# Kernel optimization log

Measured on AMD Instinct MI355X. Metric: run time of the kernel, lower is better.

The kernel has to match this reference:

```python
import jax, jax.numpy as jnp
import numpy as np

TESS = 5  # number of cells
N_POINTS = 16_777_216


def _make_basis(nc):
    # Continuity constraints of piecewise-affine velocity v(x)=a_c x + b_c at
    # interior knots x_i = i/nc:  a_i x_i + b_i - a_{i+1} x_i - b_{i+1} = 0.
    L = np.zeros((nc - 1, 2 * nc), dtype=np.float64)
    for i in range(1, nc):
        xb = i / nc
        L[i - 1, 2 * (i - 1)] = xb
        L[i - 1, 2 * (i - 1) + 1] = 1.0
        L[i - 1, 2 * i] = -xb
        L[i - 1, 2 * i + 1] = -1.0
    _, _, Vt = np.linalg.svd(L)
    B = Vt[nc - 1:].T  # (2*nc, nc+1) orthonormal null-space basis ('svd')
    return B.astype(np.float32)


def setup_inputs() -> dict:
    key = jax.random.key(0)
    k1, k2 = jax.random.split(key)
    x = jax.random.uniform(k1, (N_POINTS,), dtype=jnp.float32)
    theta = jax.random.normal(k2, (1, TESS + 1), dtype=jnp.float32) * 0.5
    B = jnp.asarray(_make_basis(TESS))
    return {"x": x, "theta": theta, "B": B}


def reference(x, theta, B):
    EPS = 1e-7
    TINY = 1e-12
    BIG = 1e10
    nc = B.shape[0] // 2
    x = jnp.clip(x, EPS, 1.0 - EPS)
    A = (B @ theta[0]).reshape(nc, 2)  # per-cell affine velocity [a_c, b_c]
    a_all, b_all = A[:, 0], A[:, 1]
    c0 = jnp.clip(jnp.floor(x * nc), 0, nc - 1).astype(jnp.int32)

    def step(carry, _):
        xc, c, t, logder = carry
        a = a_all[c]
        b = b_all[c]
        v = a * xc + b
        big = jnp.abs(a) > 1e-8
        sa = jnp.where(big, a, 1.0)
        eat = jnp.exp(a * t)
        # exact in-cell ODE solution psi(x, t)
        psi = jnp.where(big, xc * eat + (b / sa) * (eat - 1.0), xc + b * t)
        right = v >= 0
        xb = jnp.where(right, (c + 1).astype(xc.dtype), c.astype(xc.dtype)) / nc
        den = xc + b / sa
        sden = jnp.where(jnp.abs(den) > TINY, den, TINY)
        ratio = (xb + b / sa) / sden
        thit_a = jnp.log(jnp.maximum(ratio, TINY)) / sa  # time to reach boundary
        sb = jnp.where(jnp.abs(b) > TINY, b, TINY)
        thit_b = (xb - xc) / sb
        thit = jnp.where(big, thit_a, thit_b)
        valid = (jnp.abs(v) > TINY) & (thit >= 0.0) & jnp.where(big, ratio > 0.0, True)
        thit = jnp.where(valid, thit, BIG)
        hits = thit < t
        dt = jnp.where(hits, thit, t)
        x_new = jnp.where(hits, xb, psi)
        c_new = jnp.where(hits, jnp.clip(c + jnp.where(right, 1, -1), 0, nc - 1), c)
        return (x_new, c_new, t - dt, logder + a * dt), None

    init = (x, c0, jnp.ones_like(x), jnp.zeros_like(x))
    (z, _, _, logder), _ = jax.lax.scan(step, init, None, length=nc + 2)
    # log(dz/dx) = sum_c a_c * dt_c  (derivative of flow is exp of integrated slope)
    return z, logder
```

## Files before the change

### kernel.cpp

```cpp
#include <hip/hip_runtime.h>

#define NC 5
#define VEC 4


__global__ void setup_kernel(const float* __restrict__ theta,
                             const float* __restrict__ B,
                             float* __restrict__ ws)
{
    const int tid = threadIdx.x;
    const float TINY = 1e-12f, BIG = 1e10f;

    float a[NC], b[NC], bosa[NC], isa[NC], isbv[NC];
    #pragma unroll
    for (int c = 0; c < NC; ++c) {
        float av = 0.f, bv = 0.f;
        #pragma unroll
        for (int j = 0; j < 6; ++j) {
            float th = theta[j];
            av = fmaf(B[(2 * c) * 6 + j], th, av);
            bv = fmaf(B[(2 * c + 1) * 6 + j], th, bv);
        }
        const bool  big = fabsf(av) > 1e-8f;
        const float sa  = big ? av : 1.0f;
        const float sb  = (fabsf(bv) > TINY) ? bv : TINY;
        a[c] = av; b[c] = bv;
        bosa[c] = bv / sa;
        isa[c]  = 1.0f / sa;
        isbv[c] = 1.0f / sb;
    }

    if (tid < NC) {
        ws[tid * 4 + 0] = a[tid];
        ws[tid * 4 + 1] = b[tid];
        ws[tid * 4 + 2] = bosa[tid];
        ws[tid * 4 + 3] = isa[tid];
        ws[20 + tid]    = isbv[tid];
    }
    if (tid < 6) ws[25 + tid] = (float)tid / 5.0f;

    if (tid < 12) {
        const int d  = tid / 6;
        const int jb = tid % 6;
        float Ccum = 0.f, Lcum = 0.f;
        float th0 = BIG, th1 = BIG, th2 = BIG, th3 = BIG;

        for (int m = 0; m < 5; ++m) {
            const int  cf   = (d == 0) ? (jb + m) : (jb - 1 - m);
            const bool sent = (cf < 0) || (cf >= NC);
            const float xe  = (d == 0) ? ((float)cf / 5.0f)
                                       : ((float)(cf + 1) / 5.0f);
            const float af    = sent ? 0.f : a[cf];
            const float bf    = sent ? 0.f : b[cf];
            const float bosaf = sent ? 0.f : bosa[cf];

            const int pix = tid * 5 + m;
            ws[ 80 + pix * 4 + 0] = Ccum;
            ws[ 80 + pix * 4 + 1] = Lcum;
            ws[ 80 + pix * 4 + 2] = xe;
            ws[ 80 + pix * 4 + 3] = af;
            ws[320 + pix * 4 + 0] = bf;
            ws[320 + pix * 4 + 1] = bosaf;
            ws[320 + pix * 4 + 2] = 0.f;
            ws[320 + pix * 4 + 3] = 0.f;

            float T = BIG;
            if (!sent) {
                const float xL  = (float)cf / 5.0f;
                const float xR  = (float)(cf + 1) / 5.0f;
                const float xce = (d == 0) ? xL : xR;
                const float xbt = (d == 0) ? xR : xL;
                const float v   = fmaf(af, xce, bf);
                const bool  big = fabsf(af) > 1e-8f;
                const float den  = xce + bosaf;
                const float sden = (fabsf(den) > TINY) ? den : TINY;
                const float ratio = __fdividef(xbt + bosaf, sden);
                const float ta = __logf(fmaxf(ratio, TINY)) * isa[cf];
                const float tb = (xbt - xce) * isbv[cf];
                float thit = big ? ta : tb;
                const bool valid = (fabsf(v) > TINY) && (thit >= 0.f) &&
                                   (!big || (ratio > 0.f));
                T = valid ? thit : BIG;
            }
            const float newC = Ccum + T;
            if (m == 0) th0 = newC;
            if (m == 1) th1 = newC;
            if (m == 2) th2 = newC;
            if (m == 3) th3 = newC;
            if (T < BIG) Lcum = fmaf(af, T, Lcum);
            Ccum = newC;
        }
        ws[32 + tid * 4 + 0] = th0;
        ws[32 + tid * 4 + 1] = th1;
        ws[32 + tid * 4 + 2] = th2;
        ws[32 + tid * 4 + 3] = th3;
    }
}

__global__ __launch_bounds__(256) void flow_cpab_kernel(
    const float* __restrict__ x, const float* __restrict__ ws,
    float* __restrict__ out, int n)
{
    __shared__ float s[560];
    const int tid = threadIdx.x;
    if (tid < 140) ((float4*)s)[tid] = ((const float4*)ws)[tid];
    __syncthreads();

    const float4* s_k0   = (const float4*)(s);
    const float*  s_isb  = s + 20;
    const float*  s_bnd  = s + 25;
    const float4* s_thr  = (const float4*)(s + 32);
    const float4* s_pA   = (const float4*)(s + 80);
    const float4* s_pB   = (const float4*)(s + 320);

    const float EPS  = 1e-7f;
    const float TINY = 1e-12f;
    const float BIG  = 1e10f;

    const int base = (blockIdx.x * blockDim.x + tid) * VEC;
    if (base >= n) return;

    float xs[VEC], zz[VEC], ll[VEC];
    const bool full = (base + VEC <= n);
    if (full) {
        float4 xv = *(const float4*)(x + base);
        xs[0] = xv.x; xs[1] = xv.y; xs[2] = xv.z; xs[3] = xv.w;
    } else {
        for (int p = 0; p < VEC; ++p)
            xs[p] = (base + p < n) ? x[base + p] : 0.5f;
    }

    #pragma unroll
    for (int p = 0; p < VEC; ++p) {
        const float xc = fminf(fmaxf(xs[p], EPS), 1.0f - EPS);
        const int c0 = min((int)(xc * (float)NC), NC - 1);

        const float4 k0 = s_k0[c0];
        const float a = k0.x, b = k0.y, bosa = k0.z, isa = k0.w;
        const float isb = s_isb[c0];
        const bool  big = fabsf(a) > 1e-8f;

        const float v     = fmaf(a, xc, b);
        const bool  right = (v >= 0.0f);
        const int   cb    = c0 + (right ? 1 : 0);
        const float xb    = s_bnd[cb];

        const float den   = xc + bosa;
        const float sden  = (fabsf(den) > TINY) ? den : TINY;
        const float ratio = __fdividef(xb + bosa, sden);
        const float th_a  = __logf(fmaxf(ratio, TINY)) * isa;
        const float th_b  = (xb - xc) * isb;
        float thit0 = big ? th_a : th_b;
        const bool valid = (fabsf(v) > TINY) && (thit0 >= 0.0f) &&
                           (!big || (ratio > 0.0f));
        thit0 = valid ? thit0 : BIG;

        const bool  hit0 = (thit0 < 1.0f);
        const float tr   = 1.0f - thit0;

        const int tix = (right ? 0 : 6) + cb;
        const float4 th = s_thr[tix];
        const int m = (th.x < tr) + (th.y < tr) + (th.z < tr) + (th.w < tr);
        const int pix = tix * 5 + m;
        const float4 pA = s_pA[pix];
        const float4 pB = s_pB[pix];

        const float xe    = hit0 ? pA.z : xc;
        const float t_f   = hit0 ? (tr - pA.x) : 1.0f;
        const float af    = hit0 ? pA.w : a;
        const float bf    = hit0 ? pB.x : b;
        const float bosaf = hit0 ? pB.y : bosa;
        const float lbase = hit0 ? fmaf(a, thit0, pA.y) : 0.0f;

        const bool  bigf = fabsf(af) > 1e-8f;
        const float eat  = __expf(af * t_f);
        zz[p] = bigf ? fmaf(xe, eat, bosaf * (eat - 1.0f))
                     : fmaf(bf, t_f, xe);
        ll[p] = fmaf(af, t_f, lbase);
    }

    if (full) {
        *(float4*)(out + base)     = make_float4(zz[0], zz[1], zz[2], zz[3]);
        *(float4*)(out + n + base) = make_float4(ll[0], ll[1], ll[2], ll[3]);
    } else {
        for (int p = 0; p < VEC; ++p) {
            if (base + p < n) {
                out[base + p]     = zz[p];
                out[n + base + p] = ll[p];
            }
        }
    }
}

extern "C" void kernel_launch(void* const* d_in, const int* in_sizes, int n_in,
                              void* d_out, int out_size, void* d_ws, size_t ws_size,
                              hipStream_t stream) {
    const float* x     = (const float*)d_in[0];
    const float* theta = (const float*)d_in[1];
    const float* B     = (const float*)d_in[2];
    float* out = (float*)d_out;
    float* ws  = (float*)d_ws;
    const int n = in_sizes[0];

    setup_kernel<<<1, 64, 0, stream>>>(theta, B, ws);

    const int threads = 256;
    const int per_block = threads * VEC;
    const int blocks = (n + per_block - 1) / per_block;
    flow_cpab_kernel<<<blocks, threads, 0, stream>>>(x, ws, out, n);
}
```

Before: 187.7 us.

## Fuse setup into flow kernel, precompute log boundary terms, widen vector, nontemporal stores

Removes the separate one-block setup kernel: each block's first 12 threads rebuild the per-cell coefficient and prefix tables directly in shared memory, and the x loads are issued before that work so they overlap it. The first-hit time now uses a precomputed log of the boundary numerator and its sign in place of a per-point divide, so each point needs one log instead of a divide plus a log. Each thread handles 8 points instead of 4, and the outputs are written with nontemporal stores. In exchange, every block repeats the small setup computation, and there are half as many threads in flight.

```diff
diff --git a/kernel.cpp b/kernel.cpp
--- a/kernel.cpp
+++ b/kernel.cpp
@@ -1,50 +1,75 @@
 #include <hip/hip_runtime.h>
 
 #define NC 5
-#define VEC 4
+#define VEC 8
 
+typedef float fvec4 __attribute__((ext_vector_type(4)));
 
-__global__ void setup_kernel(const float* __restrict__ theta,
-                             const float* __restrict__ B,
-                             float* __restrict__ ws)
+__global__ __launch_bounds__(256) void flow_cpab_kernel(
+    const float* __restrict__ x, const float* __restrict__ theta,
+    const float* __restrict__ B, float* __restrict__ out, int n)
 {
+    __shared__ float4 s_k0[NC];
+    __shared__ float4 s_q[12];
+    __shared__ float4 s_thr[12];
+    __shared__ float4 s_pA[60];
+    __shared__ float4 s_pB[60];
+
     const int tid = threadIdx.x;
-    const float TINY = 1e-12f, BIG = 1e10f;
+    const float EPS  = 1e-7f;
+    const float TINY = 1e-12f;
+    const float BIG  = 1e10f;
+    const float LOG_TINY = -27.631021115928547f;
 
-    float a[NC], b[NC], bosa[NC], isa[NC], isbv[NC];
-    #pragma unroll
-    for (int c = 0; c < NC; ++c) {
-        float av = 0.f, bv = 0.f;
-        #pragma unroll
-        for (int j = 0; j < 6; ++j) {
-            float th = theta[j];
-            av = fmaf(B[(2 * c) * 6 + j], th, av);
-            bv = fmaf(B[(2 * c + 1) * 6 + j], th, bv);
-        }
-        const bool  big = fabsf(av) > 1e-8f;
-        const float sa  = big ? av : 1.0f;
-        const float sb  = (fabsf(bv) > TINY) ? bv : TINY;
-        a[c] = av; b[c] = bv;
-        bosa[c] = bv / sa;
-        isa[c]  = 1.0f / sa;
-        isbv[c] = 1.0f / sb;
+    const int base = (blockIdx.x * blockDim.x + tid) * VEC;
+    float xs[VEC];
+    const bool inb  = (base < n);
+    const bool full = inb && (base + VEC <= n);
+    if (full) {
+        float4 x0 = *(const float4*)(x + base);
+        float4 x1 = *(const float4*)(x + base + 4);
+        xs[0]=x0.x; xs[1]=x0.y; xs[2]=x0.z; xs[3]=x0.w;
+        xs[4]=x1.x; xs[5]=x1.y; xs[6]=x1.z; xs[7]=x1.w;
+    } else {
+        for (int p = 0; p < VEC; ++p)
+            xs[p] = (inb && base + p < n) ? x[base + p] : 0.5f;
     }
 
-    if (tid < NC) {
-        ws[tid * 4 + 0] = a[tid];
-        ws[tid * 4 + 1] = b[tid];
-        ws[tid * 4 + 2] = bosa[tid];
-        ws[tid * 4 + 3] = isa[tid];
-        ws[20 + tid]    = isbv[tid];
-    }
-    if (tid < 6) ws[25 + tid] = (float)tid / 5.0f;
+    if (tid < 12) {
+        float a[NC], b[NC], bosa[NC], isa[NC], isb[NC];
+        #pragma unroll
+        for (int c = 0; c < NC; ++c) {
+            float av = 0.f, bv = 0.f;
+            #pragma unroll
+            for (int j = 0; j < 6; ++j) {
+                float th = theta[j];
+                av = fmaf(B[(2 * c) * 6 + j], th, av);
+                bv = fmaf(B[(2 * c + 1) * 6 + j], th, bv);
+            }
+            const bool  big = fabsf(av) > 1e-8f;
+            const float sa  = big ? av : 1.0f;
+            const float sb  = (fabsf(bv) > TINY) ? bv : TINY;
+            a[c] = av; b[c] = bv;
+            bosa[c] = bv / sa; isa[c] = 1.0f / sa; isb[c] = 1.0f / sb;
+        }
+        if (tid < NC)
+            s_k0[tid] = make_float4(a[tid], b[tid], bosa[tid], isa[tid]);
 
-    if (tid < 12) {
         const int d  = tid / 6;
         const int jb = tid % 6;
+
+        {
+            const int  c0 = (d == 0) ? jb - 1 : jb;
+            const int  cs = (c0 >= 0 && c0 < NC) ? c0 : 0;
+            const float xb  = (float)jb / 5.0f;
+            const float num = xb + bosa[cs];
+            const float Lb  = __logf(fmaxf(fabsf(num), 1e-30f));
+            const float sgn = (num >= 0.f) ? 1.f : -1.f;
+            s_q[tid] = make_float4(Lb, sgn, xb, isb[cs]);
+        }
+
         float Ccum = 0.f, Lcum = 0.f;
-        float th0 = BIG, th1 = BIG, th2 = BIG, th3 = BIG;
-
+        float th[4] = {BIG, BIG, BIG, BIG};
         for (int m = 0; m < 5; ++m) {
             const int  cf   = (d == 0) ? (jb + m) : (jb - 1 - m);
             const bool sent = (cf < 0) || (cf >= NC);
@@ -53,16 +78,8 @@
             const float af    = sent ? 0.f : a[cf];
             const float bf    = sent ? 0.f : b[cf];
             const float bosaf = sent ? 0.f : bosa[cf];
-
-            const int pix = tid * 5 + m;
-            ws[ 80 + pix * 4 + 0] = Ccum;
-            ws[ 80 + pix * 4 + 1] = Lcum;
-            ws[ 80 + pix * 4 + 2] = xe;
-            ws[ 80 + pix * 4 + 3] = af;
-            ws[320 + pix * 4 + 0] = bf;
-            ws[320 + pix * 4 + 1] = bosaf;
-            ws[320 + pix * 4 + 2] = 0.f;
-            ws[320 + pix * 4 + 3] = 0.f;
+            s_pA[tid * 5 + m] = make_float4(Ccum, Lcum, xe, af);
+            s_pB[tid * 5 + m] = make_float4(bf, bosaf, 0.f, 0.f);
 
             float T = BIG;
             if (!sent) {
@@ -76,60 +93,24 @@
                 const float sden = (fabsf(den) > TINY) ? den : TINY;
                 const float ratio = __fdividef(xbt + bosaf, sden);
                 const float ta = __logf(fmaxf(ratio, TINY)) * isa[cf];
-                const float tb = (xbt - xce) * isbv[cf];
+                const float tb = (xbt - xce) * isb[cf];
                 float thit = big ? ta : tb;
                 const bool valid = (fabsf(v) > TINY) && (thit >= 0.f) &&
                                    (!big || (ratio > 0.f));
                 T = valid ? thit : BIG;
             }
             const float newC = Ccum + T;
-            if (m == 0) th0 = newC;
-            if (m == 1) th1 = newC;
-            if (m == 2) th2 = newC;
-            if (m == 3) th3 = newC;
+            if (m < 4) th[m] = newC;
             if (T < BIG) Lcum = fmaf(af, T, Lcum);
             Ccum = newC;
         }
-        ws[32 + tid * 4 + 0] = th0;
-        ws[32 + tid * 4 + 1] = th1;
-        ws[32 + tid * 4 + 2] = th2;
-        ws[32 + tid * 4 + 3] = th3;
+        s_thr[tid] = make_float4(th[0], th[1], th[2], th[3]);
     }
-}
-
-__global__ __launch_bounds__(256) void flow_cpab_kernel(
-    const float* __restrict__ x, const float* __restrict__ ws,
-    float* __restrict__ out, int n)
-{
-    __shared__ float s[560];
-    const int tid = threadIdx.x;
-    if (tid < 140) ((float4*)s)[tid] = ((const float4*)ws)[tid];
     __syncthreads();
 
-    const float4* s_k0   = (const float4*)(s);
-    const float*  s_isb  = s + 20;
-    const float*  s_bnd  = s + 25;
-    const float4* s_thr  = (const float4*)(s + 32);
-    const float4* s_pA   = (const float4*)(s + 80);
-    const float4* s_pB   = (const float4*)(s + 320);
+    if (!inb) return;
 
-    const float EPS  = 1e-7f;
-    const float TINY = 1e-12f;
-    const float BIG  = 1e10f;
-
-    const int base = (blockIdx.x * blockDim.x + tid) * VEC;
-    if (base >= n) return;
-
-    float xs[VEC], zz[VEC], ll[VEC];
-    const bool full = (base + VEC <= n);
-    if (full) {
-        float4 xv = *(const float4*)(x + base);
-        xs[0] = xv.x; xs[1] = xv.y; xs[2] = xv.z; xs[3] = xv.w;
-    } else {
-        for (int p = 0; p < VEC; ++p)
-            xs[p] = (base + p < n) ? x[base + p] : 0.5f;
-    }
-
+    float zz[VEC], ll[VEC];
     #pragma unroll
     for (int p = 0; p < VEC; ++p) {
         const float xc = fminf(fmaxf(xs[p], EPS), 1.0f - EPS);
@@ -137,28 +118,26 @@
 
         const float4 k0 = s_k0[c0];
         const float a = k0.x, b = k0.y, bosa = k0.z, isa = k0.w;
-        const float isb = s_isb[c0];
         const bool  big = fabsf(a) > 1e-8f;
 
         const float v     = fmaf(a, xc, b);
         const bool  right = (v >= 0.0f);
-        const int   cb    = c0 + (right ? 1 : 0);
-        const float xb    = s_bnd[cb];
+        const int   tix   = (right ? 0 : 6) + c0 + (right ? 1 : 0);
+        const float4 q    = s_q[tix];
 
-        const float den   = xc + bosa;
-        const float sden  = (fabsf(den) > TINY) ? den : TINY;
-        const float ratio = __fdividef(xb + bosa, sden);
-        const float th_a  = __logf(fmaxf(ratio, TINY)) * isa;
-        const float th_b  = (xb - xc) * isb;
+        const float den  = xc + bosa;
+        const float l    = __logf(fmaxf(fabsf(den), TINY));
+        const float diff = fmaxf(q.x - l, LOG_TINY);
+        const float th_a = diff * isa;
+        const float th_b = (q.z - xc) * q.w;
         float thit0 = big ? th_a : th_b;
         const bool valid = (fabsf(v) > TINY) && (thit0 >= 0.0f) &&
-                           (!big || (ratio > 0.0f));
+                           (!big || (den * q.y > 0.0f));
         thit0 = valid ? thit0 : BIG;
 
         const bool  hit0 = (thit0 < 1.0f);
         const float tr   = 1.0f - thit0;
 
-        const int tix = (right ? 0 : 6) + cb;
         const float4 th = s_thr[tix];
         const int m = (th.x < tr) + (th.y < tr) + (th.z < tr) + (th.w < tr);
         const int pix = tix * 5 + m;
@@ -180,8 +159,14 @@
     }
 
     if (full) {
-        *(float4*)(out + base)     = make_float4(zz[0], zz[1], zz[2], zz[3]);
-        *(float4*)(out + n + base) = make_float4(ll[0], ll[1], ll[2], ll[3]);
+        fvec4 z0 = {zz[0], zz[1], zz[2], zz[3]};
+        fvec4 z1 = {zz[4], zz[5], zz[6], zz[7]};
+        fvec4 l0 = {ll[0], ll[1], ll[2], ll[3]};
+        fvec4 l1 = {ll[4], ll[5], ll[6], ll[7]};
+        __builtin_nontemporal_store(z0, (fvec4*)(out + base));
+        __builtin_nontemporal_store(z1, (fvec4*)(out + base + 4));
+        __builtin_nontemporal_store(l0, (fvec4*)(out + n + base));
+        __builtin_nontemporal_store(l1, (fvec4*)(out + n + base + 4));
     } else {
         for (int p = 0; p < VEC; ++p) {
             if (base + p < n) {
@@ -199,13 +184,10 @@
     const float* theta = (const float*)d_in[1];
     const float* B     = (const float*)d_in[2];
     float* out = (float*)d_out;
-    float* ws  = (float*)d_ws;
     const int n = in_sizes[0];
-
-    setup_kernel<<<1, 64, 0, stream>>>(theta, B, ws);
 
     const int threads = 256;
     const int per_block = threads * VEC;
     const int blocks = (n + per_block - 1) / per_block;
-    flow_cpab_kernel<<<blocks, threads, 0, stream>>>(x, ws, out, n);
+    flow_cpab_kernel<<<blocks, threads, 0, stream>>>(x, theta, B, out, n);
 }
```

Result: slower. 194.7 us (+3.7%).
